# Kernel tuning notes

Measured on AMD Instinct MI355X. Metric: run time of the kernel, lower is better.

The kernel has to match this reference:

```python
import jax, jax.numpy as jnp
import numpy as np

N_NODES = 100000
N_EDGES = 640000
IN_FEATS = 128
OUT_FEATS = 128


def setup_inputs() -> dict:
    key = jax.random.key(0)
    k1, k2, k3, k4 = jax.random.split(key, 4)
    feature = jax.random.normal(k1, (N_NODES, IN_FEATS), dtype=jnp.float32)
    edge_index = jax.random.randint(k2, (2, N_EDGES), 0, N_NODES, dtype=jnp.int64)
    # Linear params (W stored as [in, out] so out = h @ W + b, same math as torch Linear)
    W = jax.random.normal(k3, (IN_FEATS, OUT_FEATS), dtype=jnp.float32) / np.sqrt(IN_FEATS)
    b = jax.random.normal(k4, (OUT_FEATS,), dtype=jnp.float32) * 0.01
    return {"feature": feature, "edge_index": edge_index, "W": W, "b": b}


def reference(feature, edge_index, W, b):
    src, dst = edge_index[0], edge_index[1]
    # copy_src: gather source-node features along edges -> [E, in]
    msgs = feature[src]
    # sum reduce at destination nodes -> [N, in]
    h = jax.ops.segment_sum(msgs, dst, num_segments=N_NODES)
    # post-aggregation linear
    return h @ W + b
```

## Files before the change

kernel.cpp:

```cpp
#include <hip/hip_runtime.h>

#define N_NODES 100000
#define N_EDGES 640000
#define FEATS   128
#define CAP     32

typedef __attribute__((ext_vector_type(8))) short short8;
typedef __attribute__((ext_vector_type(4))) float f32x4;

static __device__ __forceinline__ unsigned short f2bf(float f) {
  union { float f; unsigned u; } c; c.f = f;
  unsigned u = c.u + 0x7fffu + ((c.u >> 16) & 1u);
  return (unsigned short)(u >> 16);
}
static __device__ __forceinline__ float asf(unsigned u) {
  union { unsigned u; float f; } c; c.u = u;
  return c.f;
}

__global__ __launch_bounds__(256) void fused_prep(
    const float* __restrict__ feature, const float* __restrict__ W,
    const int* __restrict__ edge,
    unsigned short* __restrict__ feat_bf, unsigned short* __restrict__ WT,
    int* __restrict__ cnt, int* __restrict__ bucket) {
  int b = blockIdx.x;
  if (b < 6250) {
    size_t g = (size_t)b * 256 + threadIdx.x;
    const float4* s = (const float4*)feature + g * 2;
    float4 a = s[0], c = s[1];
    unsigned short o[8] = {f2bf(a.x), f2bf(a.y), f2bf(a.z), f2bf(a.w),
                           f2bf(c.x), f2bf(c.y), f2bf(c.z), f2bf(c.w)};
    *(short8*)(feat_bf + g * 8) = *(const short8*)o;
  } else if (b < 6314) {
    int g = (b - 6250) * 256 + threadIdx.x;
    int k = g >> 7, n = g & 127;
    WT[n * 128 + k] = f2bf(W[g]);
  } else {
    int t    = b - 6314;
    int cls  = t & 7;
    int base = (t >> 3) * 2048;
    #pragma unroll
    for (int k = 0; k < 8; ++k) {
      int e = base + k * 256 + threadIdx.x;
      if (e < N_EDGES) {
        int d = edge[N_EDGES + e];
        if (((d >> 4) & 7) == cls) {
          int s = edge[e];
          int slot = atomicAdd(&cnt[d], 1);
          if (slot < CAP) bucket[slot * N_NODES + d] = s;
        }
      }
    }
  }
}

__global__ __launch_bounds__(256) void aggregate_kernel(
    const unsigned short* __restrict__ feat,
    const int* __restrict__ cnt, const int* __restrict__ bucket,
    unsigned short* __restrict__ h) {
  int g    = blockIdx.x * 256 + threadIdx.x;
  int node = g >> 4;
  int lane = g & 15;
  int deg  = min(cnt[node], CAP);
  const int* eb = bucket + node;

  float a0 = 0.f, a1 = 0.f, a2 = 0.f, a3 = 0.f;
  float a4 = 0.f, a5 = 0.f, a6 = 0.f, a7 = 0.f;

  int i = 0;
  for (; i + 3 < deg; i += 4) {
    int s0 = eb[(size_t)(i + 0) * N_NODES];
    int s1 = eb[(size_t)(i + 1) * N_NODES];
    int s2 = eb[(size_t)(i + 2) * N_NODES];
    int s3 = eb[(size_t)(i + 3) * N_NODES];
    uint4 p0 = *(const uint4*)(feat + (size_t)s0 * FEATS + lane * 8);
    uint4 p1 = *(const uint4*)(feat + (size_t)s1 * FEATS + lane * 8);
    uint4 p2 = *(const uint4*)(feat + (size_t)s2 * FEATS + lane * 8);
    uint4 p3 = *(const uint4*)(feat + (size_t)s3 * FEATS + lane * 8);
    a0 += asf(p0.x << 16) + asf(p1.x << 16) + asf(p2.x << 16) + asf(p3.x << 16);
    a1 += asf(p0.x & 0xffff0000u) + asf(p1.x & 0xffff0000u) + asf(p2.x & 0xffff0000u) + asf(p3.x & 0xffff0000u);
    a2 += asf(p0.y << 16) + asf(p1.y << 16) + asf(p2.y << 16) + asf(p3.y << 16);
    a3 += asf(p0.y & 0xffff0000u) + asf(p1.y & 0xffff0000u) + asf(p2.y & 0xffff0000u) + asf(p3.y & 0xffff0000u);
    a4 += asf(p0.z << 16) + asf(p1.z << 16) + asf(p2.z << 16) + asf(p3.z << 16);
    a5 += asf(p0.z & 0xffff0000u) + asf(p1.z & 0xffff0000u) + asf(p2.z & 0xffff0000u) + asf(p3.z & 0xffff0000u);
    a6 += asf(p0.w << 16) + asf(p1.w << 16) + asf(p2.w << 16) + asf(p3.w << 16);
    a7 += asf(p0.w & 0xffff0000u) + asf(p1.w & 0xffff0000u) + asf(p2.w & 0xffff0000u) + asf(p3.w & 0xffff0000u);
  }
  for (; i < deg; ++i) {
    int s = eb[(size_t)i * N_NODES];
    uint4 p = *(const uint4*)(feat + (size_t)s * FEATS + lane * 8);
    a0 += asf(p.x << 16);
    a1 += asf(p.x & 0xffff0000u);
    a2 += asf(p.y << 16);
    a3 += asf(p.y & 0xffff0000u);
    a4 += asf(p.z << 16);
    a5 += asf(p.z & 0xffff0000u);
    a6 += asf(p.w << 16);
    a7 += asf(p.w & 0xffff0000u);
  }

  uint4 o;
  o.x = (unsigned)f2bf(a0) | ((unsigned)f2bf(a1) << 16);
  o.y = (unsigned)f2bf(a2) | ((unsigned)f2bf(a3) << 16);
  o.z = (unsigned)f2bf(a4) | ((unsigned)f2bf(a5) << 16);
  o.w = (unsigned)f2bf(a6) | ((unsigned)f2bf(a7) << 16);
  *(uint4*)(h + (size_t)node * FEATS + lane * 8) = o;
}


#define LDSK 136

__global__ __launch_bounds__(256) void gemm_mfma(
    const unsigned short* __restrict__ hbf,
    const unsigned short* __restrict__ WT,
    const float* __restrict__ bias,
    float* __restrict__ out) {
  __shared__ unsigned short WTs[128 * LDSK];

  #pragma unroll
  for (int i = 0; i < 8; ++i) {
    int c = threadIdx.x + i * 256;
    int n = c >> 4, j = c & 15;
    *(short8*)&WTs[n * LDSK + j * 8] = *(const short8*)(WT + n * 128 + j * 8);
  }
  __syncthreads();

  const int w    = threadIdx.x >> 6;
  const int lane = threadIdx.x & 63;
  const int ln15 = lane & 15;
  const int quad = lane >> 4;
  const int row_base = blockIdx.x * 128 + w * 32;

  f32x4 acc[2][8] = {};

  #pragma unroll
  for (int kb = 0; kb < 4; ++kb) {
    int kofs = kb * 32 + quad * 8;
    short8 a0 = *(const short8*)(hbf + (size_t)(row_base + ln15) * FEATS + kofs);
    short8 a1 = *(const short8*)(hbf + (size_t)(row_base + 16 + ln15) * FEATS + kofs);
    #pragma unroll
    for (int ct = 0; ct < 8; ++ct) {
      short8 b = *(const short8*)&WTs[(ct * 16 + ln15) * LDSK + kofs];
      acc[0][ct] = __builtin_amdgcn_mfma_f32_16x16x32_bf16(a0, b, acc[0][ct], 0, 0, 0);
      acc[1][ct] = __builtin_amdgcn_mfma_f32_16x16x32_bf16(a1, b, acc[1][ct], 0, 0, 0);
    }
  }

  #pragma unroll
  for (int t = 0; t < 2; ++t) {
    #pragma unroll
    for (int ct = 0; ct < 8; ++ct) {
      int col = ct * 16 + ln15;
      float bv = bias[col];
      #pragma unroll
      for (int r = 0; r < 4; ++r) {
        int row = row_base + t * 16 + quad * 4 + r;
        if (row < N_NODES)
          __builtin_nontemporal_store(acc[t][ct][r] + bv,
                                      &out[(size_t)row * FEATS + col]);
      }
    }
  }
}


extern "C" void kernel_launch(void* const* d_in, const int* in_sizes, int n_in,
                              void* d_out, int out_size, void* d_ws, size_t ws_size,
                              hipStream_t stream) {
  const float* feature = (const float*)d_in[0];
  const int*   edge    = (const int*)d_in[1];
  const float* W       = (const float*)d_in[2];
  const float* bias    = (const float*)d_in[3];
  float*       out     = (float*)d_out;

  char* ws = (char*)d_ws;
  int* cnt    = (int*)(ws);
  int* bucket = (int*)(ws + (1 << 20));
  unsigned short* WT      = (unsigned short*)(ws + (27 << 20));
  unsigned short* feat_bf = (unsigned short*)(ws + (28 << 20));
  unsigned short* h_bf    = (unsigned short*)(ws + (54 << 20));

  hipMemsetAsync(cnt, 0, N_NODES * sizeof(int), stream);

  fused_prep<<<6314 + 313 * 8, 256, 0, stream>>>(
      feature, W, edge, feat_bf, WT, cnt, bucket);

  aggregate_kernel<<<N_NODES * 16 / 256, 256, 0, stream>>>(
      feat_bf, cnt, bucket, h_bf);

  gemm_mfma<<<(N_NODES + 127) / 128, 256, 0, stream>>>(h_bf, WT, bias, out);
}
```

Measured before the change: 181.7 us.

## Fuse aggregation into GEMM kernel, staging aggregated rows in swizzled LDS

Merges the aggregation and GEMM kernels into one kernel. Each block aggregates 128 nodes into shared memory and then runs the MFMA GEMM on that tile, so the bf16 h intermediate no longer goes to global memory and one launch is removed. LDS tiles switch from padded to XOR-swizzled layout. The cost is a smaller grid (782 blocks instead of 6250) with 64KB of LDS per block, which lowers occupancy and the number of gathers in flight during the latency-bound gather phase.

```diff
diff --git a/kernel.cpp b/kernel.cpp
--- a/kernel.cpp
+++ b/kernel.cpp
@@ -7,6 +7,8 @@
 
 typedef __attribute__((ext_vector_type(8))) short short8;
 typedef __attribute__((ext_vector_type(4))) float f32x4;
+
+#define SWZ(row, kofs) (((row) << 7) + ((((kofs) >> 3) ^ ((row) & 7)) << 3))
 
 static __device__ __forceinline__ unsigned short f2bf(float f) {
   union { float f; unsigned u; } c; c.f = f;
@@ -54,75 +56,72 @@
   }
 }
 
-__global__ __launch_bounds__(256) void aggregate_kernel(
+__global__ __launch_bounds__(256) void agg_gemm(
     const unsigned short* __restrict__ feat,
     const int* __restrict__ cnt, const int* __restrict__ bucket,
-    unsigned short* __restrict__ h) {
-  int g    = blockIdx.x * 256 + threadIdx.x;
-  int node = g >> 4;
-  int lane = g & 15;
-  int deg  = min(cnt[node], CAP);
-  const int* eb = bucket + node;
-
-  float a0 = 0.f, a1 = 0.f, a2 = 0.f, a3 = 0.f;
-  float a4 = 0.f, a5 = 0.f, a6 = 0.f, a7 = 0.f;
-
-  int i = 0;
-  for (; i + 3 < deg; i += 4) {
-    int s0 = eb[(size_t)(i + 0) * N_NODES];
-    int s1 = eb[(size_t)(i + 1) * N_NODES];
-    int s2 = eb[(size_t)(i + 2) * N_NODES];
-    int s3 = eb[(size_t)(i + 3) * N_NODES];
-    uint4 p0 = *(const uint4*)(feat + (size_t)s0 * FEATS + lane * 8);
-    uint4 p1 = *(const uint4*)(feat + (size_t)s1 * FEATS + lane * 8);
-    uint4 p2 = *(const uint4*)(feat + (size_t)s2 * FEATS + lane * 8);
-    uint4 p3 = *(const uint4*)(feat + (size_t)s3 * FEATS + lane * 8);
-    a0 += asf(p0.x << 16) + asf(p1.x << 16) + asf(p2.x << 16) + asf(p3.x << 16);
-    a1 += asf(p0.x & 0xffff0000u) + asf(p1.x & 0xffff0000u) + asf(p2.x & 0xffff0000u) + asf(p3.x & 0xffff0000u);
-    a2 += asf(p0.y << 16) + asf(p1.y << 16) + asf(p2.y << 16) + asf(p3.y << 16);
-    a3 += asf(p0.y & 0xffff0000u) + asf(p1.y & 0xffff0000u) + asf(p2.y & 0xffff0000u) + asf(p3.y & 0xffff0000u);
-    a4 += asf(p0.z << 16) + asf(p1.z << 16) + asf(p2.z << 16) + asf(p3.z << 16);
-    a5 += asf(p0.z & 0xffff0000u) + asf(p1.z & 0xffff0000u) + asf(p2.z & 0xffff0000u) + asf(p3.z & 0xffff0000u);
-    a6 += asf(p0.w << 16) + asf(p1.w << 16) + asf(p2.w << 16) + asf(p3.w << 16);
-    a7 += asf(p0.w & 0xffff0000u) + asf(p1.w & 0xffff0000u) + asf(p2.w & 0xffff0000u) + asf(p3.w & 0xffff0000u);
-  }
-  for (; i < deg; ++i) {
-    int s = eb[(size_t)i * N_NODES];
-    uint4 p = *(const uint4*)(feat + (size_t)s * FEATS + lane * 8);
-    a0 += asf(p.x << 16);
-    a1 += asf(p.x & 0xffff0000u);
-    a2 += asf(p.y << 16);
-    a3 += asf(p.y & 0xffff0000u);
-    a4 += asf(p.z << 16);
-    a5 += asf(p.z & 0xffff0000u);
-    a6 += asf(p.w << 16);
-    a7 += asf(p.w & 0xffff0000u);
-  }
-
-  uint4 o;
-  o.x = (unsigned)f2bf(a0) | ((unsigned)f2bf(a1) << 16);
-  o.y = (unsigned)f2bf(a2) | ((unsigned)f2bf(a3) << 16);
-  o.z = (unsigned)f2bf(a4) | ((unsigned)f2bf(a5) << 16);
-  o.w = (unsigned)f2bf(a6) | ((unsigned)f2bf(a7) << 16);
-  *(uint4*)(h + (size_t)node * FEATS + lane * 8) = o;
-}
-
-
-#define LDSK 136
-
-__global__ __launch_bounds__(256) void gemm_mfma(
-    const unsigned short* __restrict__ hbf,
     const unsigned short* __restrict__ WT,
     const float* __restrict__ bias,
     float* __restrict__ out) {
-  __shared__ unsigned short WTs[128 * LDSK];
+  __shared__ unsigned short WTs[128 * 128];
+  __shared__ unsigned short hs[128 * 128];
 
   #pragma unroll
   for (int i = 0; i < 8; ++i) {
     int c = threadIdx.x + i * 256;
     int n = c >> 4, j = c & 15;
-    *(short8*)&WTs[n * LDSK + j * 8] = *(const short8*)(WT + n * 128 + j * 8);
+    *(short8*)&WTs[SWZ(n, j * 8)] = *(const short8*)(WT + n * 128 + j * 8);
   }
+
+  #pragma unroll
+  for (int it = 0; it < 8; ++it) {
+    int l    = it * 16 + (threadIdx.x >> 4);
+    int node = blockIdx.x * 128 + l;
+    int lane = threadIdx.x & 15;
+
+    float a0 = 0.f, a1 = 0.f, a2 = 0.f, a3 = 0.f;
+    float a4 = 0.f, a5 = 0.f, a6 = 0.f, a7 = 0.f;
+
+    if (node < N_NODES) {
+      int deg = min(cnt[node], CAP);
+      const int* eb = bucket + node;
+      int i = 0;
+      for (; i + 3 < deg; i += 4) {
+        int s0 = eb[(size_t)(i + 0) * N_NODES];
+        int s1 = eb[(size_t)(i + 1) * N_NODES];
+        int s2 = eb[(size_t)(i + 2) * N_NODES];
+        int s3 = eb[(size_t)(i + 3) * N_NODES];
+        uint4 p0 = *(const uint4*)(feat + (size_t)s0 * FEATS + lane * 8);
+        uint4 p1 = *(const uint4*)(feat + (size_t)s1 * FEATS + lane * 8);
+        uint4 p2 = *(const uint4*)(feat + (size_t)s2 * FEATS + lane * 8);
+        uint4 p3 = *(const uint4*)(feat + (size_t)s3 * FEATS + lane * 8);
+        a0 += asf(p0.x << 16) + asf(p1.x << 16) + asf(p2.x << 16) + asf(p3.x << 16);
+        a1 += asf(p0.x & 0xffff0000u) + asf(p1.x & 0xffff0000u) + asf(p2.x & 0xffff0000u) + asf(p3.x & 0xffff0000u);
+        a2 += asf(p0.y << 16) + asf(p1.y << 16) + asf(p2.y << 16) + asf(p3.y << 16);
+        a3 += asf(p0.y & 0xffff0000u) + asf(p1.y & 0xffff0000u) + asf(p2.y & 0xffff0000u) + asf(p3.y & 0xffff0000u);
+        a4 += asf(p0.z << 16) + asf(p1.z << 16) + asf(p2.z << 16) + asf(p3.z << 16);
+        a5 += asf(p0.z & 0xffff0000u) + asf(p1.z & 0xffff0000u) + asf(p2.z & 0xffff0000u) + asf(p3.z & 0xffff0000u);
+        a6 += asf(p0.w << 16) + asf(p1.w << 16) + asf(p2.w << 16) + asf(p3.w << 16);
+        a7 += asf(p0.w & 0xffff0000u) + asf(p1.w & 0xffff0000u) + asf(p2.w & 0xffff0000u) + asf(p3.w & 0xffff0000u);
+      }
+      for (; i < deg; ++i) {
+        int s = eb[(size_t)i * N_NODES];
+        uint4 p = *(const uint4*)(feat + (size_t)s * FEATS + lane * 8);
+        a0 += asf(p.x << 16);
+        a1 += asf(p.x & 0xffff0000u);
+        a2 += asf(p.y << 16);
+        a3 += asf(p.y & 0xffff0000u);
+        a4 += asf(p.z << 16);
+        a5 += asf(p.z & 0xffff0000u);
+        a6 += asf(p.w << 16);
+        a7 += asf(p.w & 0xffff0000u);
+      }
+    }
+
+    unsigned short o[8] = {f2bf(a0), f2bf(a1), f2bf(a2), f2bf(a3),
+                           f2bf(a4), f2bf(a5), f2bf(a6), f2bf(a7)};
+    *(short8*)&hs[SWZ(l, lane * 8)] = *(const short8*)o;
+  }
+
   __syncthreads();
 
   const int w    = threadIdx.x >> 6;
@@ -136,11 +135,12 @@
   #pragma unroll
   for (int kb = 0; kb < 4; ++kb) {
     int kofs = kb * 32 + quad * 8;
-    short8 a0 = *(const short8*)(hbf + (size_t)(row_base + ln15) * FEATS + kofs);
-    short8 a1 = *(const short8*)(hbf + (size_t)(row_base + 16 + ln15) * FEATS + kofs);
+    int r0 = w * 32 + ln15;
+    short8 a0 = *(const short8*)&hs[SWZ(r0, kofs)];
+    short8 a1 = *(const short8*)&hs[SWZ(r0 + 16, kofs)];
     #pragma unroll
     for (int ct = 0; ct < 8; ++ct) {
-      short8 b = *(const short8*)&WTs[(ct * 16 + ln15) * LDSK + kofs];
+      short8 b = *(const short8*)&WTs[SWZ(ct * 16 + ln15, kofs)];
       acc[0][ct] = __builtin_amdgcn_mfma_f32_16x16x32_bf16(a0, b, acc[0][ct], 0, 0, 0);
       acc[1][ct] = __builtin_amdgcn_mfma_f32_16x16x32_bf16(a1, b, acc[1][ct], 0, 0, 0);
     }
@@ -178,15 +178,12 @@
   int* bucket = (int*)(ws + (1 << 20));
   unsigned short* WT      = (unsigned short*)(ws + (27 << 20));
   unsigned short* feat_bf = (unsigned short*)(ws + (28 << 20));
-  unsigned short* h_bf    = (unsigned short*)(ws + (54 << 20));
 
   hipMemsetAsync(cnt, 0, N_NODES * sizeof(int), stream);
 
   fused_prep<<<6314 + 313 * 8, 256, 0, stream>>>(
       feature, W, edge, feat_bf, WT, cnt, bucket);
 
-  aggregate_kernel<<<N_NODES * 16 / 256, 256, 0, stream>>>(
-      feat_bf, cnt, bucket, h_bf);
-
-  gemm_mfma<<<(N_NODES + 127) / 128, 256, 0, stream>>>(h_bf, WT, bias, out);
+  agg_gemm<<<(N_NODES + 127) / 128, 256, 0, stream>>>(
+      feat_bf, cnt, bucket, WT, bias, out);
 }
```

Result: slower. 203.6 us (+12.0%).
